# Performance work log

Measured on AMD Instinct MI355X. Metric: run time of the kernel, lower is better.

## Reference

```python
import jax, jax.numpy as jnp
import numpy as np

P_DROP = 0.1

def setup_inputs() -> dict:
    key = jax.random.key(0)
    kq, kk, kv, km = jax.random.split(key, 4)
    B, H, S, D = 2, 16, 2048, 128
    q = jax.random.normal(kq, (B, H, S, D), dtype=jnp.float32)
    k = jax.random.normal(kk, (B, H, S, D), dtype=jnp.float32)
    v = jax.random.normal(kv, (B, H, S, D), dtype=jnp.float32)
    # Deterministic inverted-dropout mask: keep with prob 1-p, scaled by 1/(1-p)
    keep = jax.random.bernoulli(km, 1.0 - P_DROP, (B, H, S, S))
    drop_mask = keep.astype(jnp.float32) / jnp.float32(1.0 - P_DROP)
    return {"q": q, "k": k, "v": v, "drop_mask": drop_mask}

def reference(q, k, v, drop_mask):
    # qk: [B,H,S,S] = q @ k^T (no softmax, per the original module)
    qk = jnp.einsum("bhsd,bhtd->bhst", q, k)
    dropped = qk * drop_mask  # inverted dropout, p=0.1
    out = jnp.einsum("bhst,bhtd->bhsd", dropped, v)
    return out
```

## Files before the change

kernel.cpp:

```cpp
#include <hip/hip_runtime.h>

#define S_LEN 2048
#define D_DIM 128
#define BM 128
#define BK 64
#define NIT (S_LEN / BK)
#define LQ 136
#define LV 72

typedef __attribute__((ext_vector_type(8))) short bf16x8;
typedef __attribute__((ext_vector_type(4))) float f32x4;
typedef __attribute__((ext_vector_type(4))) int i32x4;

__device__ __forceinline__ unsigned short f2bf(float x) {
    union { float f; unsigned u; } c; c.f = x;
    unsigned r = c.u + 0x7fffu + ((c.u >> 16) & 1u);
    return (unsigned short)(r >> 16);
}
__device__ __forceinline__ unsigned pack2(float a, float b) {
    return (unsigned)f2bf(a) | ((unsigned)f2bf(b) << 16);
}

__global__ __launch_bounds__(256, 2)
void fused_qkmv(const float* __restrict__ q, const float* __restrict__ k,
                const float* __restrict__ v, const float* __restrict__ mask,
                float* __restrict__ out) {
    __shared__ unsigned short Qs[BM * LQ];
    __shared__ unsigned short Ks[BK * LQ];
    __shared__ unsigned short Vt[D_DIM * LV];

    const int tid  = threadIdx.x;
    const int lane = tid & 63;
    const int w    = tid >> 6;
    const int l15  = lane & 15;
    const int qd   = lane >> 4;

    const int bh = blockIdx.x >> 4;
    const int s0 = (blockIdx.x & 15) * BM;

    const float* qp = q + (size_t)bh * S_LEN * D_DIM;
    const float* kp = k + (size_t)bh * S_LEN * D_DIM;
    const float* vp = v + (size_t)bh * S_LEN * D_DIM;
    const float* mp = mask + (size_t)bh * S_LEN * S_LEN;
    float*       op = out + (size_t)bh * S_LEN * D_DIM;

    {
        const int r = tid >> 5, d = (tid & 31) * 4;
#pragma unroll
        for (int sw = 0; sw < 16; ++sw) {
            const int row = sw * 8 + r;
            float4 f = *(const float4*)(qp + (size_t)(s0 + row) * D_DIM + d);
            uint2 wv; wv.x = pack2(f.x, f.y); wv.y = pack2(f.z, f.w);
            *(uint2*)&Qs[row * LQ + d] = wv;
        }
    }

    f32x4 acc_o[2][8];
#pragma unroll
    for (int i = 0; i < 2; ++i)
#pragma unroll
        for (int j = 0; j < 8; ++j) acc_o[i][j] = (f32x4){0.f, 0.f, 0.f, 0.f};

    const int a0 = ((2 * (qd & 1)) * 16 + l15) * 4;
    const int a1 = a0 + 64;
    const bool hi = (qd >= 2);

    for (int it = 0; it < NIT; ++it) {
        const int t0 = it * BK;

        float4 mreg[4][2];
        {
            const float* mb = mp + (size_t)(s0 + 32 * w + l15) * S_LEN + t0 + 4 * qd;
#pragma unroll
            for (int ti = 0; ti < 4; ++ti)
#pragma unroll
                for (int sj = 0; sj < 2; ++sj)
                    mreg[ti][sj] = *(const float4*)(mb + (size_t)sj * 16 * S_LEN + ti * 16);
        }

        {
            const int tk = tid >> 2, dk = (tid & 3) * 4;
            float4 f[8];
#pragma unroll
            for (int i = 0; i < 8; ++i)
                f[i] = *(const float4*)(kp + (size_t)(t0 + tk) * D_DIM + dk + 16 * i);
#pragma unroll
            for (int i = 0; i < 8; ++i) {
                uint2 wv; wv.x = pack2(f[i].x, f[i].y); wv.y = pack2(f[i].z, f[i].w);
                *(uint2*)&Ks[tk * LQ + dk + 16 * i] = wv;
            }
        }
        {
            const int tg = (tid & 15) * 4, dg = (tid >> 4) * 8;
            float4 ra[4], rb[4];
#pragma unroll
            for (int r = 0; r < 4; ++r) {
                ra[r] = *(const float4*)(vp + (size_t)(t0 + tg + r) * D_DIM + dg);
                rb[r] = *(const float4*)(vp + (size_t)(t0 + tg + r) * D_DIM + dg + 4);
            }
#pragma unroll
            for (int i = 0; i < 4; ++i) {
                uint2 wv;
                wv.x = pack2(((const float*)&ra[0])[i], ((const float*)&ra[1])[i]);
                wv.y = pack2(((const float*)&ra[2])[i], ((const float*)&ra[3])[i]);
                *(uint2*)&Vt[(dg + i) * LV + tg] = wv;
                uint2 wv2;
                wv2.x = pack2(((const float*)&rb[0])[i], ((const float*)&rb[1])[i]);
                wv2.y = pack2(((const float*)&rb[2])[i], ((const float*)&rb[3])[i]);
                *(uint2*)&Vt[(dg + 4 + i) * LV + tg] = wv2;
            }
        }

        f32x4 acc_s[4][2];
#pragma unroll
        for (int i = 0; i < 4; ++i)
#pragma unroll
            for (int j = 0; j < 2; ++j) acc_s[i][j] = (f32x4){0.f, 0.f, 0.f, 0.f};

        __syncthreads();

#pragma unroll
        for (int kc = 0; kc < 4; ++kc) {
            const int ko = kc * 32 + qd * 8;
            bf16x8 af[4], bq[2];
#pragma unroll
            for (int ti = 0; ti < 4; ++ti)
                af[ti] = *(const bf16x8*)&Ks[(16 * ti + l15) * LQ + ko];
#pragma unroll
            for (int sj = 0; sj < 2; ++sj)
                bq[sj] = *(const bf16x8*)&Qs[(32 * w + 16 * sj + l15) * LQ + ko];
#pragma unroll
            for (int ti = 0; ti < 4; ++ti)
#pragma unroll
                for (int sj = 0; sj < 2; ++sj)
                    acc_s[ti][sj] = __builtin_amdgcn_mfma_f32_16x16x32_bf16(
                        af[ti], bq[sj], acc_s[ti][sj], 0, 0, 0);
        }

        int pu[4][2][2];
#pragma unroll
        for (int ti = 0; ti < 4; ++ti)
#pragma unroll
            for (int sj = 0; sj < 2; ++sj) {
                f32x4 sv = acc_s[ti][sj];
                float4 m = mreg[ti][sj];
                pu[ti][sj][0] = (int)pack2(sv[0] * m.x, sv[1] * m.y);
                pu[ti][sj][1] = (int)pack2(sv[2] * m.z, sv[3] * m.w);
            }

#pragma unroll
        for (int kc2 = 0; kc2 < 2; ++kc2) {
            bf16x8 ap[2];
#pragma unroll
            for (int sj = 0; sj < 2; ++sj) {
                const int tA = 2 * kc2, tB = 2 * kc2 + 1;
                int w0a = __builtin_amdgcn_ds_bpermute(a0, pu[tA][sj][0]);
                int w0b = __builtin_amdgcn_ds_bpermute(a0, pu[tB][sj][0]);
                int w1a = __builtin_amdgcn_ds_bpermute(a0, pu[tA][sj][1]);
                int w1b = __builtin_amdgcn_ds_bpermute(a0, pu[tB][sj][1]);
                int w2a = __builtin_amdgcn_ds_bpermute(a1, pu[tA][sj][0]);
                int w2b = __builtin_amdgcn_ds_bpermute(a1, pu[tB][sj][0]);
                int w3a = __builtin_amdgcn_ds_bpermute(a1, pu[tA][sj][1]);
                int w3b = __builtin_amdgcn_ds_bpermute(a1, pu[tB][sj][1]);
                union { i32x4 i; bf16x8 b; } u;
                u.i = (i32x4){hi ? w0b : w0a, hi ? w1b : w1a,
                              hi ? w2b : w2a, hi ? w3b : w3a};
                ap[sj] = u.b;
            }
            const int ko = kc2 * 32 + qd * 8;
#pragma unroll
            for (int dj = 0; dj < 8; ++dj) {
                bf16x8 bv = *(const bf16x8*)&Vt[(16 * dj + l15) * LV + ko];
#pragma unroll
                for (int si = 0; si < 2; ++si)
                    acc_o[si][dj] = __builtin_amdgcn_mfma_f32_16x16x32_bf16(
                        ap[si], bv, acc_o[si][dj], 0, 0, 0);
            }
        }

        __syncthreads();
    }

#pragma unroll
    for (int si = 0; si < 2; ++si)
#pragma unroll
        for (int dj = 0; dj < 8; ++dj) {
#pragma unroll
            for (int r = 0; r < 4; ++r) {
                const int srow = s0 + 32 * w + 16 * si + 4 * qd + r;
                op[(size_t)srow * D_DIM + 16 * dj + l15] = acc_o[si][dj][r];
            }
        }
}

extern "C" void kernel_launch(void* const* d_in, const int* in_sizes, int n_in,
                              void* d_out, int out_size, void* d_ws, size_t ws_size,
                              hipStream_t stream) {
    const float* q = (const float*)d_in[0];
    const float* k = (const float*)d_in[1];
    const float* v = (const float*)d_in[2];
    const float* m = (const float*)d_in[3];
    float* out = (float*)d_out;
    fused_qkmv<<<dim3(512), dim3(256), 0, stream>>>(q, k, v, m, out);
}
```

Before: 806.2 us.

## Double-buffer K/V tiles with register prefetch and keep Q in registers

K and V tiles now use double-buffered LDS, with the next tile's K, V and mask loaded into registers during the current tile's MFMA work, leaving one barrier per iteration. Q fragments stay in registers as bf16 instead of in LDS. Software bf16 rounding is replaced by the v_cvt_pk_bf16_f32 instruction, and block indices are remapped to spread heads across groups. This hides global-load latency behind compute, at the cost of more register pressure that could hurt occupancy at two blocks per CU.

Measured after the change: 806.4 us. Within noise of the previous version (+0.0%).

```diff
diff --git a/kernel.cpp b/kernel.cpp
--- a/kernel.cpp
+++ b/kernel.cpp
@@ -12,22 +12,26 @@
 typedef __attribute__((ext_vector_type(4))) float f32x4;
 typedef __attribute__((ext_vector_type(4))) int i32x4;
 
-__device__ __forceinline__ unsigned short f2bf(float x) {
-    union { float f; unsigned u; } c; c.f = x;
-    unsigned r = c.u + 0x7fffu + ((c.u >> 16) & 1u);
-    return (unsigned short)(r >> 16);
-}
-__device__ __forceinline__ unsigned pack2(float a, float b) {
-    return (unsigned)f2bf(a) | ((unsigned)f2bf(b) << 16);
+__device__ __forceinline__ unsigned cvtpk(float lo, float hi) {
+    unsigned r;
+    asm("v_cvt_pk_bf16_f32 %0, %1, %2" : "=v"(r) : "v"(lo), "v"(hi));
+    return r;
+}
+__device__ __forceinline__ bf16x8 pack8(float4 a, float4 b) {
+    union { unsigned u[4]; bf16x8 v; } r;
+    r.u[0] = cvtpk(a.x, a.y);
+    r.u[1] = cvtpk(a.z, a.w);
+    r.u[2] = cvtpk(b.x, b.y);
+    r.u[3] = cvtpk(b.z, b.w);
+    return r.v;
 }
 
 __global__ __launch_bounds__(256, 2)
 void fused_qkmv(const float* __restrict__ q, const float* __restrict__ k,
                 const float* __restrict__ v, const float* __restrict__ mask,
                 float* __restrict__ out) {
-    __shared__ unsigned short Qs[BM * LQ];
-    __shared__ unsigned short Ks[BK * LQ];
-    __shared__ unsigned short Vt[D_DIM * LV];
+    __shared__ __align__(16) unsigned short Ks[2][BK * LQ];
+    __shared__ __align__(16) unsigned short Vt[2][D_DIM * LV];
 
     const int tid  = threadIdx.x;
     const int lane = tid & 63;
@@ -35,8 +39,10 @@
     const int l15  = lane & 15;
     const int qd   = lane >> 4;
 
-    const int bh = blockIdx.x >> 4;
-    const int s0 = (blockIdx.x & 15) * BM;
+    const int bid = (int)blockIdx.x;
+    const int wg  = (bid & 7) * 64 + (bid >> 3);
+    const int bh  = wg >> 4;
+    const int s0  = (wg & 15) * BM;
 
     const float* qp = q + (size_t)bh * S_LEN * D_DIM;
     const float* kp = k + (size_t)bh * S_LEN * D_DIM;
@@ -44,14 +50,42 @@
     const float* mp = mask + (size_t)bh * S_LEN * S_LEN;
     float*       op = out + (size_t)bh * S_LEN * D_DIM;
 
-    {
-        const int r = tid >> 5, d = (tid & 31) * 4;
-#pragma unroll
-        for (int sw = 0; sw < 16; ++sw) {
-            const int row = sw * 8 + r;
-            float4 f = *(const float4*)(qp + (size_t)(s0 + row) * D_DIM + d);
-            uint2 wv; wv.x = pack2(f.x, f.y); wv.y = pack2(f.z, f.w);
-            *(uint2*)&Qs[row * LQ + d] = wv;
+    const int tk = tid >> 2;
+    const int ck = (tid & 3) * 8;
+    const int tg = (tid & 15) * 4;
+    const int dg = (tid >> 4) * 8;
+
+    float4 kr[8], va[4], vbr[4];
+#pragma unroll
+    for (int i = 0; i < 4; ++i) {
+        const float* kb = kp + (size_t)tk * D_DIM + ck + 32 * i;
+        kr[2 * i]     = *(const float4*)kb;
+        kr[2 * i + 1] = *(const float4*)(kb + 4);
+    }
+#pragma unroll
+    for (int r = 0; r < 4; ++r) {
+        const float* vb = vp + (size_t)(tg + r) * D_DIM + dg;
+        va[r]  = *(const float4*)vb;
+        vbr[r] = *(const float4*)(vb + 4);
+    }
+
+    const float* mbase = mp + (size_t)(s0 + 32 * w + l15) * S_LEN + 4 * qd;
+    float4 mreg[4][2];
+#pragma unroll
+    for (int ti = 0; ti < 4; ++ti)
+#pragma unroll
+        for (int sj = 0; sj < 2; ++sj)
+            mreg[ti][sj] = *(const float4*)(mbase + (size_t)sj * 16 * S_LEN + ti * 16);
+
+    bf16x8 qreg[2][4];
+#pragma unroll
+    for (int sj = 0; sj < 2; ++sj) {
+        const float* qb = qp + (size_t)(s0 + 32 * w + 16 * sj + l15) * D_DIM + qd * 8;
+#pragma unroll
+        for (int kc = 0; kc < 4; ++kc) {
+            float4 f0 = *(const float4*)(qb + kc * 32);
+            float4 f1 = *(const float4*)(qb + kc * 32 + 4);
+            qreg[sj][kc] = pack8(f0, f1);
         }
     }
 
@@ -65,50 +99,39 @@
     const int a1 = a0 + 64;
     const bool hi = (qd >= 2);
 
+#pragma unroll 2
     for (int it = 0; it < NIT; ++it) {
-        const int t0 = it * BK;
-
-        float4 mreg[4][2];
-        {
-            const float* mb = mp + (size_t)(s0 + 32 * w + l15) * S_LEN + t0 + 4 * qd;
-#pragma unroll
-            for (int ti = 0; ti < 4; ++ti)
-#pragma unroll
-                for (int sj = 0; sj < 2; ++sj)
-                    mreg[ti][sj] = *(const float4*)(mb + (size_t)sj * 16 * S_LEN + ti * 16);
-        }
-
-        {
-            const int tk = tid >> 2, dk = (tid & 3) * 4;
-            float4 f[8];
-#pragma unroll
-            for (int i = 0; i < 8; ++i)
-                f[i] = *(const float4*)(kp + (size_t)(t0 + tk) * D_DIM + dk + 16 * i);
-#pragma unroll
-            for (int i = 0; i < 8; ++i) {
-                uint2 wv; wv.x = pack2(f[i].x, f[i].y); wv.y = pack2(f[i].z, f[i].w);
-                *(uint2*)&Ks[tk * LQ + dk + 16 * i] = wv;
-            }
-        }
-        {
-            const int tg = (tid & 15) * 4, dg = (tid >> 4) * 8;
-            float4 ra[4], rb[4];
-#pragma unroll
-            for (int r = 0; r < 4; ++r) {
-                ra[r] = *(const float4*)(vp + (size_t)(t0 + tg + r) * D_DIM + dg);
-                rb[r] = *(const float4*)(vp + (size_t)(t0 + tg + r) * D_DIM + dg + 4);
-            }
-#pragma unroll
-            for (int i = 0; i < 4; ++i) {
-                uint2 wv;
-                wv.x = pack2(((const float*)&ra[0])[i], ((const float*)&ra[1])[i]);
-                wv.y = pack2(((const float*)&ra[2])[i], ((const float*)&ra[3])[i]);
-                *(uint2*)&Vt[(dg + i) * LV + tg] = wv;
-                uint2 wv2;
-                wv2.x = pack2(((const float*)&rb[0])[i], ((const float*)&rb[1])[i]);
-                wv2.y = pack2(((const float*)&rb[2])[i], ((const float*)&rb[3])[i]);
-                *(uint2*)&Vt[(dg + 4 + i) * LV + tg] = wv2;
-            }
+        const int cur = it & 1;
+        const int t0n = ((it + 1) & (NIT - 1)) * BK;
+
+#pragma unroll
+        for (int i = 0; i < 4; ++i)
+            *(bf16x8*)&Ks[cur][tk * LQ + ck + 32 * i] = pack8(kr[2 * i], kr[2 * i + 1]);
+#pragma unroll
+        for (int i = 0; i < 4; ++i) {
+            uint2 w0, w1;
+            w0.x = cvtpk(((const float*)&va[0])[i], ((const float*)&va[1])[i]);
+            w0.y = cvtpk(((const float*)&va[2])[i], ((const float*)&va[3])[i]);
+            *(uint2*)&Vt[cur][(dg + i) * LV + tg] = w0;
+            w1.x = cvtpk(((const float*)&vbr[0])[i], ((const float*)&vbr[1])[i]);
+            w1.y = cvtpk(((const float*)&vbr[2])[i], ((const float*)&vbr[3])[i]);
+            *(uint2*)&Vt[cur][(dg + 4 + i) * LV + tg] = w1;
+        }
+
+        asm volatile("s_waitcnt lgkmcnt(0)" ::: "memory");
+        __builtin_amdgcn_s_barrier();
+
+#pragma unroll
+        for (int i = 0; i < 4; ++i) {
+            const float* kb = kp + (size_t)(t0n + tk) * D_DIM + ck + 32 * i;
+            kr[2 * i]     = *(const float4*)kb;
+            kr[2 * i + 1] = *(const float4*)(kb + 4);
+        }
+#pragma unroll
+        for (int r = 0; r < 4; ++r) {
+            const float* vb = vp + (size_t)(t0n + tg + r) * D_DIM + dg;
+            va[r]  = *(const float4*)vb;
+            vbr[r] = *(const float4*)(vb + 4);
         }
 
         f32x4 acc_s[4][2];
@@ -116,25 +139,19 @@
         for (int i = 0; i < 4; ++i)
 #pragma unroll
             for (int j = 0; j < 2; ++j) acc_s[i][j] = (f32x4){0.f, 0.f, 0.f, 0.f};
-
-        __syncthreads();
-
 #pragma unroll
         for (int kc = 0; kc < 4; ++kc) {
             const int ko = kc * 32 + qd * 8;
-            bf16x8 af[4], bq[2];
+            bf16x8 af[4];
 #pragma unroll
             for (int ti = 0; ti < 4; ++ti)
-                af[ti] = *(const bf16x8*)&Ks[(16 * ti + l15) * LQ + ko];
-#pragma unroll
-            for (int sj = 0; sj < 2; ++sj)
-                bq[sj] = *(const bf16x8*)&Qs[(32 * w + 16 * sj + l15) * LQ + ko];
+                af[ti] = *(const bf16x8*)&Ks[cur][(16 * ti + l15) * LQ + ko];
 #pragma unroll
             for (int ti = 0; ti < 4; ++ti)
 #pragma unroll
                 for (int sj = 0; sj < 2; ++sj)
                     acc_s[ti][sj] = __builtin_amdgcn_mfma_f32_16x16x32_bf16(
-                        af[ti], bq[sj], acc_s[ti][sj], 0, 0, 0);
+                        af[ti], qreg[sj][kc], acc_s[ti][sj], 0, 0, 0);
         }
 
         int pu[4][2][2];
@@ -144,9 +161,15 @@
             for (int sj = 0; sj < 2; ++sj) {
                 f32x4 sv = acc_s[ti][sj];
                 float4 m = mreg[ti][sj];
-                pu[ti][sj][0] = (int)pack2(sv[0] * m.x, sv[1] * m.y);
-                pu[ti][sj][1] = (int)pack2(sv[2] * m.z, sv[3] * m.w);
-            }
+                pu[ti][sj][0] = (int)cvtpk(sv[0] * m.x, sv[1] * m.y);
+                pu[ti][sj][1] = (int)cvtpk(sv[2] * m.z, sv[3] * m.w);
+            }
+
+#pragma unroll
+        for (int ti = 0; ti < 4; ++ti)
+#pragma unroll
+            for (int sj = 0; sj < 2; ++sj)
+                mreg[ti][sj] = *(const float4*)(mbase + t0n + (size_t)sj * 16 * S_LEN + ti * 16);
 
 #pragma unroll
         for (int kc2 = 0; kc2 < 2; ++kc2) {
@@ -170,15 +193,13 @@
             const int ko = kc2 * 32 + qd * 8;
 #pragma unroll
             for (int dj = 0; dj < 8; ++dj) {
-                bf16x8 bv = *(const bf16x8*)&Vt[(16 * dj + l15) * LV + ko];
+                bf16x8 bv = *(const bf16x8*)&Vt[cur][(16 * dj + l15) * LV + ko];
 #pragma unroll
                 for (int si = 0; si < 2; ++si)
                     acc_o[si][dj] = __builtin_amdgcn_mfma_f32_16x16x32_bf16(
                         ap[si], bv, acc_o[si][dj], 0, 0, 0);
             }
         }
-
-        __syncthreads();
     }
 
 #pragma unroll
```
